# Optimization experiments

Hardware: AMD Instinct MI355X
Metric: run time of the kernel (lower is better)

Reference implementation:

```python
import jax, jax.numpy as jnp
import numpy as np

WINDOW_SIZE = 11
SIGMA = 1.5
C1 = 0.01 ** 2
C2 = 0.03 ** 2
ALPHA = 0.84


def _gaussian_window(window_size, sigma):
    x = np.arange(window_size, dtype=np.float32)
    g = np.exp(-((x - window_size // 2) ** 2) / (2.0 * sigma ** 2))
    g = g / g.sum()
    w2d = np.outer(g, g).astype(np.float32)  # [K, K]
    return jnp.asarray(w2d)


def _depthwise_conv(x, window):
    # x: [B, C, H, W]; window: [K, K] shared across channels (depthwise)
    C = x.shape[1]
    K = window.shape[0]
    kern = jnp.broadcast_to(window[None, None], (C, 1, K, K))  # [C, 1, K, K] OIHW
    pad = K // 2
    return jax.lax.conv_general_dilated(
        x, kern,
        window_strides=(1, 1),
        padding=((pad, pad), (pad, pad)),
        dimension_numbers=('NCHW', 'OIHW', 'NCHW'),
        feature_group_count=C,
    )


def _ssim(img1, img2):
    window = _gaussian_window(WINDOW_SIZE, SIGMA)
    mu1 = _depthwise_conv(img1, window)
    mu2 = _depthwise_conv(img2, window)
    mu1_sq = mu1 * mu1
    mu2_sq = mu2 * mu2
    mu1_mu2 = mu1 * mu2
    sigma1_sq = _depthwise_conv(img1 * img1, window) - mu1_sq
    sigma2_sq = _depthwise_conv(img2 * img2, window) - mu2_sq
    sigma12 = _depthwise_conv(img1 * img2, window) - mu1_mu2
    ssim_map = ((2 * mu1_mu2 + C1) * (2 * sigma12 + C2)) / (
        (mu1_sq + mu2_sq + C1) * (sigma1_sq + sigma2_sq + C2))
    return ssim_map.mean()


def setup_inputs() -> dict:
    key = jax.random.key(0)
    k1, k2 = jax.random.split(key)
    shape = (32, 3, 512, 512)
    pred = jax.random.uniform(k1, shape, dtype=jnp.float32)
    target = jax.random.uniform(k2, shape, dtype=jnp.float32)
    return {"pred": pred, "target": target}


def reference(pred, target):
    l1 = jnp.mean(jnp.abs(pred - target))
    s = _ssim(pred, target)
    return ALPHA * l1 + (1.0 - ALPHA) * (1.0 - s)
```

## Files before the change

kernel.cpp:

```cpp
#include <hip/hip_runtime.h>

#define SSIM_H 512
#define SSIM_W 512
#define PLANES 96
#define TILE_W 64
#define TILE_H 32
#define GRID_X (SSIM_W / TILE_W)
#define GRID_Y (SSIM_H / TILE_H)
#define TOTAL_BLOCKS (GRID_X * GRID_Y * PLANES)
#define N_TOTAL 25165824.0

typedef _Float16 half4v __attribute__((ext_vector_type(4)));
typedef _Float16 half8v __attribute__((ext_vector_type(8)));
typedef float float4v __attribute__((ext_vector_type(4)));

struct __align__(8) f2 { float x, y; };

__device__ __forceinline__ float gwf(int k) {
  const float d = (float)(k - 5);
  return __expf(-d * d / 4.5f) * 0.26601171702936207f;
}

__global__ __launch_bounds__(256, 7)
void ssim_l1_kernel(const float* __restrict__ pred,
                    const float* __restrict__ targ,
                    f2* __restrict__ partials) {
  __shared__ _Float16 Hs[4][64][44];
  __shared__ float red[2][4];

  const int tid = (int)threadIdx.x;
  const int wv = tid >> 6;
  const int lane = tid & 63;
  const int q = lane >> 4;
  const int m = lane & 15;

  const int tr0 = (int)blockIdx.y * TILE_H;
  const int tc0 = (int)blockIdx.x * TILE_W;
  const size_t pbase = (size_t)blockIdx.z * (SSIM_H * SSIM_W);
  const float* __restrict__ xp = pred + pbase;
  const float* __restrict__ yp = targ + pbase;

  half8v wf;
#pragma unroll
  for (int j = 0; j < 8; ++j) {
    const int k = 8 * q + j - m;
    const float v = (k >= 0 && k <= 10) ? gwf(k) : 0.0f;
    wf[j] = (_Float16)v;
  }

  const int cw = tc0 + 16 * wv;
  const int cbase = cw - 5 + 8 * q;
  const bool cfast = (cbase >= 0) && (cbase + 7 < SSIM_W);

  float l1 = 0.0f;

#pragma unroll
  for (int rg = 0; rg < 3; ++rg) {
    const int grow = tr0 - 5 + rg * 16 + m;
    float xf[8], yf[8];
    if ((unsigned)grow < (unsigned)SSIM_H) {
      const float* __restrict__ xr = xp + (size_t)grow * SSIM_W;
      const float* __restrict__ yr = yp + (size_t)grow * SSIM_W;
      if (cfast) {
        float4 a0, a1, b0, b1;
        __builtin_memcpy(&a0, xr + cbase, 16);
        __builtin_memcpy(&a1, xr + cbase + 4, 16);
        __builtin_memcpy(&b0, yr + cbase, 16);
        __builtin_memcpy(&b1, yr + cbase + 4, 16);
        xf[0] = a0.x; xf[1] = a0.y; xf[2] = a0.z; xf[3] = a0.w;
        xf[4] = a1.x; xf[5] = a1.y; xf[6] = a1.z; xf[7] = a1.w;
        yf[0] = b0.x; yf[1] = b0.y; yf[2] = b0.z; yf[3] = b0.w;
        yf[4] = b1.x; yf[5] = b1.y; yf[6] = b1.z; yf[7] = b1.w;
      } else {
#pragma unroll
        for (int j = 0; j < 8; ++j) {
          const int c = cbase + j;
          const bool ok = (unsigned)c < (unsigned)SSIM_W;
          xf[j] = ok ? xr[c] : 0.0f;
          yf[j] = ok ? yr[c] : 0.0f;
        }
      }
    } else {
#pragma unroll
      for (int j = 0; j < 8; ++j) { xf[j] = 0.0f; yf[j] = 0.0f; }
    }

    const int hr = rg * 16 + m;
    if (hr >= 5 && hr < 5 + TILE_H) {
#pragma unroll
      for (int j = 0; j < 8; ++j) {
        const int k = 8 * q + j;
        if (k >= 5 && k < 21) l1 += fabsf(xf[j] - yf[j]);
      }
    }

    half8v ax, ay, axxyy, axy;
#pragma unroll
    for (int j = 0; j < 8; ++j) {
      const float x = xf[j], y = yf[j];
      ax[j]    = (_Float16)x;
      ay[j]    = (_Float16)y;
      axxyy[j] = (_Float16)(x * x + y * y);
      axy[j]   = (_Float16)(x * y);
    }
    const float4v z = {0.0f, 0.0f, 0.0f, 0.0f};
    float4v c0 = __builtin_amdgcn_mfma_f32_16x16x32_f16(ax,    wf, z, 0, 0, 0);
    float4v c1 = __builtin_amdgcn_mfma_f32_16x16x32_f16(ay,    wf, z, 0, 0, 0);
    float4v c2 = __builtin_amdgcn_mfma_f32_16x16x32_f16(axxyy, wf, z, 0, 0, 0);
    float4v c3 = __builtin_amdgcn_mfma_f32_16x16x32_f16(axy,   wf, z, 0, 0, 0);

    if (rg != 2 || q != 3) {
      const int hcol = 16 * wv + m;
      const int hrow = rg * 16 + 4 * q;
      half4v h;
      h[0] = (_Float16)c0[0]; h[1] = (_Float16)c0[1];
      h[2] = (_Float16)c0[2]; h[3] = (_Float16)c0[3];
      *(half4v*)&Hs[0][hcol][hrow] = h;
      h[0] = (_Float16)c1[0]; h[1] = (_Float16)c1[1];
      h[2] = (_Float16)c1[2]; h[3] = (_Float16)c1[3];
      *(half4v*)&Hs[1][hcol][hrow] = h;
      h[0] = (_Float16)c2[0]; h[1] = (_Float16)c2[1];
      h[2] = (_Float16)c2[2]; h[3] = (_Float16)c2[3];
      *(half4v*)&Hs[2][hcol][hrow] = h;
      h[0] = (_Float16)c3[0]; h[1] = (_Float16)c3[1];
      h[2] = (_Float16)c3[2]; h[3] = (_Float16)c3[3];
      *(half4v*)&Hs[3][hcol][hrow] = h;
    }
  }

  asm volatile("s_waitcnt lgkmcnt(0)" ::: "memory");
  __builtin_amdgcn_sched_barrier(0);

  float ssim = 0.0f;
  {
    const int hcol = 16 * wv + m;
    half8v bfr[2][4];
#pragma unroll
    for (int rb = 0; rb < 2; ++rb) {
      const int hrow = 16 * rb + 8 * q;
      const int hrow_hi = (hrow + 4 <= 40) ? hrow + 4 : 40;
#pragma unroll
      for (int p = 0; p < 4; ++p) {
        half4v lo = *(const half4v*)&Hs[p][hcol][hrow];
        half4v hi = *(const half4v*)&Hs[p][hcol][hrow_hi];
        bfr[rb][p] = __builtin_shufflevector(lo, hi, 0, 1, 2, 3, 4, 5, 6, 7);
      }
    }
    const float C1v = 1.0e-4f, C2v = 9.0e-4f;
#pragma unroll
    for (int rb = 0; rb < 2; ++rb) {
      const float4v z = {0.0f, 0.0f, 0.0f, 0.0f};
      float4v acc[4];
#pragma unroll
      for (int p = 0; p < 4; ++p)
        acc[p] = __builtin_amdgcn_mfma_f32_16x16x32_f16(wf, bfr[rb][p], z,
                                                        0, 0, 0);
#pragma unroll
      for (int r = 0; r < 4; ++r) {
        const float mu1 = acc[0][r], mu2 = acc[1][r];
        const float exxyy = acc[2][r], exy = acc[3][r];
        const float m11 = mu1 * mu1, m22 = mu2 * mu2, m12 = mu1 * mu2;
        const float num = (2.0f * m12 + C1v) * (2.0f * (exy - m12) + C2v);
        const float den = (m11 + m22 + C1v) *
                          ((exxyy - m11 - m22) + C2v);
        ssim += num / den;
      }
    }
  }

  float v0 = l1, v1 = ssim;
#pragma unroll
  for (int off = 32; off > 0; off >>= 1) {
    v0 += __shfl_down(v0, off, 64);
    v1 += __shfl_down(v1, off, 64);
  }
  if (lane == 0) { red[0][wv] = v0; red[1][wv] = v1; }
  __syncthreads();
  if (tid == 0) {
    f2 s;
    s.x = red[0][0] + red[0][1] + red[0][2] + red[0][3];
    s.y = red[1][0] + red[1][1] + red[1][2] + red[1][3];
    const int bid = ((int)blockIdx.z * GRID_Y + (int)blockIdx.y) * GRID_X +
                    (int)blockIdx.x;
    partials[bid] = s;
  }
}

__global__ __launch_bounds__(256)
void finalize_kernel(const f2* __restrict__ partials,
                     float* __restrict__ out) {
  __shared__ double red[2][4];
  const int tid = (int)threadIdx.x;
  double L = 0.0, S = 0.0;
  for (int i = tid; i < TOTAL_BLOCKS; i += 256) {
    const f2 v = partials[i];
    L += (double)v.x;
    S += (double)v.y;
  }
#pragma unroll
  for (int off = 32; off > 0; off >>= 1) {
    L += __shfl_down(L, off, 64);
    S += __shfl_down(S, off, 64);
  }
  const int lane = tid & 63, wid = tid >> 6;
  if (lane == 0) { red[0][wid] = L; red[1][wid] = S; }
  __syncthreads();
  if (tid == 0) {
    const double Ls = red[0][0] + red[0][1] + red[0][2] + red[0][3];
    const double Ss = red[1][0] + red[1][1] + red[1][2] + red[1][3];
    const double invN = 1.0 / N_TOTAL;
    out[0] = (float)(0.84 * (Ls * invN) + 0.16 * (1.0 - Ss * invN));
  }
}

extern "C" void kernel_launch(void* const* d_in, const int* in_sizes, int n_in,
                              void* d_out, int out_size, void* d_ws, size_t ws_size,
                              hipStream_t stream) {
  const float* pred = (const float*)d_in[0];
  const float* targ = (const float*)d_in[1];
  float* out = (float*)d_out;
  f2* partials = (f2*)d_ws;

  dim3 grid(GRID_X, GRID_Y, PLANES);
  ssim_l1_kernel<<<grid, 256, 0, stream>>>(pred, targ, partials);
  finalize_kernel<<<1, 256, 0, stream>>>(partials, out);
}
```

Before: 264.7 us.

## Stage raw input tiles into LDS with coalesced dwordx4 loads before convolution

The kernel now loads the 44x84 halo tiles of both images cooperatively into shared memory with aligned 16-byte global loads and clamped addresses. The per-lane MFMA operands are then read from LDS, with edge masking applied only on boundary blocks. This replaces the old per-lane unaligned global loads that re-fetched overlapping halo data. In exchange it adds about 30 KB of LDS per block and a barrier, and lowers the launch-bounds occupancy hint from 7 to 3.

```diff
diff --git a/kernel.cpp b/kernel.cpp
--- a/kernel.cpp
+++ b/kernel.cpp
@@ -10,6 +10,12 @@
 #define TOTAL_BLOCKS (GRID_X * GRID_Y * PLANES)
 #define N_TOTAL 25165824.0
 
+#define RAW_ROWS 44
+#define RAW_STRIDE 86
+#define RAW_CHUNKS (2 * RAW_ROWS * 21)
+#define STG_FULL (RAW_CHUNKS / 256)
+#define STG_TAIL (RAW_CHUNKS - STG_FULL * 256)
+
 typedef _Float16 half4v __attribute__((ext_vector_type(4)));
 typedef _Float16 half8v __attribute__((ext_vector_type(8)));
 typedef float float4v __attribute__((ext_vector_type(4)));
@@ -21,10 +27,11 @@
   return __expf(-d * d / 4.5f) * 0.26601171702936207f;
 }
 
-__global__ __launch_bounds__(256, 7)
+__global__ __launch_bounds__(256, 3)
 void ssim_l1_kernel(const float* __restrict__ pred,
                     const float* __restrict__ targ,
                     f2* __restrict__ partials) {
+  __shared__ float Raw[2][RAW_ROWS][RAW_STRIDE];
   __shared__ _Float16 Hs[4][64][44];
   __shared__ float red[2][4];
 
@@ -40,6 +47,39 @@
   const float* __restrict__ xp = pred + pbase;
   const float* __restrict__ yp = targ + pbase;
 
+  float4v stg[8];
+  int doff[8];
+#pragma unroll
+  for (int k = 0; k < 8; ++k) {
+    if (k < STG_FULL || tid < STG_TAIL) {
+      const int c = k * 256 + tid;
+      const int row = c / 42;
+      const int rem = c - row * 42;
+      const int img = rem / 21;
+      const int pos = rem - img * 21;
+      const int gr = min(max(tr0 - 5 + row, 0), SSIM_H - 1);
+      const int gc = min(max(tc0 - 8 + 4 * pos, 0), SSIM_W - 4);
+      const float* src = (img ? yp : xp) + ((size_t)gr << 9) + gc;
+      asm volatile("global_load_dwordx4 %0, %1, off"
+                   : "=v"(stg[k]) : "v"(src) : "memory");
+      doff[k] = (img * RAW_ROWS + row) * RAW_STRIDE + 4 * pos;
+    }
+  }
+  asm volatile("s_waitcnt vmcnt(0)" ::: "memory");
+  __builtin_amdgcn_sched_barrier(0);
+#pragma unroll
+  for (int k = 0; k < 8; ++k) {
+    if (k < STG_FULL || tid < STG_TAIL) {
+      float* d = &Raw[0][0][0] + doff[k];
+      f2 lo, hi;
+      lo.x = stg[k][0]; lo.y = stg[k][1];
+      hi.x = stg[k][2]; hi.y = stg[k][3];
+      *(f2*)d = lo;
+      *(f2*)(d + 2) = hi;
+    }
+  }
+  __syncthreads();
+
   half8v wf;
 #pragma unroll
   for (int j = 0; j < 8; ++j) {
@@ -50,43 +90,49 @@
 
   const int cw = tc0 + 16 * wv;
   const int cbase = cw - 5 + 8 * q;
-  const bool cfast = (cbase >= 0) && (cbase + 7 < SSIM_W);
+  const int o = 16 * wv + 8 * q + 3;
+  const bool xedge = (tc0 == 0) || (tc0 == SSIM_W - TILE_W);
+  const bool yedge = (tr0 == 0) || (tr0 == SSIM_H - TILE_H);
 
   float l1 = 0.0f;
 
 #pragma unroll
   for (int rg = 0; rg < 3; ++rg) {
-    const int grow = tr0 - 5 + rg * 16 + m;
-    float xf[8], yf[8];
-    if ((unsigned)grow < (unsigned)SSIM_H) {
-      const float* __restrict__ xr = xp + (size_t)grow * SSIM_W;
-      const float* __restrict__ yr = yp + (size_t)grow * SSIM_W;
-      if (cfast) {
-        float4 a0, a1, b0, b1;
-        __builtin_memcpy(&a0, xr + cbase, 16);
-        __builtin_memcpy(&a1, xr + cbase + 4, 16);
-        __builtin_memcpy(&b0, yr + cbase, 16);
-        __builtin_memcpy(&b1, yr + cbase + 4, 16);
-        xf[0] = a0.x; xf[1] = a0.y; xf[2] = a0.z; xf[3] = a0.w;
-        xf[4] = a1.x; xf[5] = a1.y; xf[6] = a1.z; xf[7] = a1.w;
-        yf[0] = b0.x; yf[1] = b0.y; yf[2] = b0.z; yf[3] = b0.w;
-        yf[4] = b1.x; yf[5] = b1.y; yf[6] = b1.z; yf[7] = b1.w;
-      } else {
-#pragma unroll
-        for (int j = 0; j < 8; ++j) {
-          const int c = cbase + j;
-          const bool ok = (unsigned)c < (unsigned)SSIM_W;
-          xf[j] = ok ? xr[c] : 0.0f;
-          yf[j] = ok ? yr[c] : 0.0f;
-        }
-      }
-    } else {
-#pragma unroll
-      for (int j = 0; j < 8; ++j) { xf[j] = 0.0f; yf[j] = 0.0f; }
-    }
-
-    const int hr = rg * 16 + m;
-    if (hr >= 5 && hr < 5 + TILE_H) {
+    const int r = rg * 16 + m;
+    const int rs = r < 43 ? r : 43;
+    const float* Rx = &Raw[0][rs][0];
+    const float* Ry = &Raw[1][rs][0];
+    f2 a0 = *(const f2*)(Rx + o - 1);
+    f2 a1 = *(const f2*)(Rx + o + 1);
+    f2 a2 = *(const f2*)(Rx + o + 3);
+    f2 a3 = *(const f2*)(Rx + o + 5);
+    float a4 = Rx[o + 7];
+    f2 b0 = *(const f2*)(Ry + o - 1);
+    f2 b1 = *(const f2*)(Ry + o + 1);
+    f2 b2 = *(const f2*)(Ry + o + 3);
+    f2 b3 = *(const f2*)(Ry + o + 5);
+    float b4 = Ry[o + 7];
+    float xf[8] = {a0.y, a1.x, a1.y, a2.x, a2.y, a3.x, a3.y, a4};
+    float yf[8] = {b0.y, b1.x, b1.y, b2.x, b2.y, b3.x, b3.y, b4};
+
+    if (yedge) {
+      const bool okr = (unsigned)(tr0 - 5 + r) < (unsigned)SSIM_H;
+#pragma unroll
+      for (int j = 0; j < 8; ++j) {
+        xf[j] = okr ? xf[j] : 0.0f;
+        yf[j] = okr ? yf[j] : 0.0f;
+      }
+    }
+    if (xedge) {
+#pragma unroll
+      for (int j = 0; j < 8; ++j) {
+        const bool ok = (unsigned)(cbase + j) < (unsigned)SSIM_W;
+        xf[j] = ok ? xf[j] : 0.0f;
+        yf[j] = ok ? yf[j] : 0.0f;
+      }
+    }
+
+    if (r >= 5 && r < 5 + TILE_H) {
 #pragma unroll
       for (int j = 0; j < 8; ++j) {
         const int k = 8 * q + j;
```

Result: no change. 262.3 us (-0.9%).
